# Optimization experiments

Measured on AMD Instinct MI355X. Metric: run time of the kernel, lower is better.

## Reference

```python
import jax, jax.numpy as jnp
import numpy as np

DT = 600.0          # integration time step (s)
STEPS = 20          # number of Euler steps
R_EARTH = 6371000.0
DEG2RAD = np.pi / 180.0
KERNEL = jnp.array([[1.0, 2.0, 1.0], [2.0, 4.0, 2.0], [1.0, 2.0, 1.0]], dtype=jnp.float32) / 16.0


def setup_inputs() -> dict:
    key = jax.random.key(0)
    kT, ku, kv, km = jax.random.split(key, 4)
    B, H, W = 8, 360, 720  # 0.5-degree global grid
    T = jax.random.normal(kT, (B, H, W), dtype=jnp.float32)
    ug = jax.random.normal(ku, (B, H, W), dtype=jnp.float32) * 0.5
    vg = jax.random.normal(kv, (B, H, W), dtype=jnp.float32) * 0.5
    lat = (90.0 - 0.25 - jnp.arange(H, dtype=jnp.float32) * 0.5)
    lon = jnp.arange(W, dtype=jnp.float32) * 0.5
    mask = (jax.random.uniform(km, (H, W)) > 0.3).astype(jnp.float32)  # ocean mask
    return {"T": T, "ug": ug, "vg": vg, "lat": lat, "lon": lon, "mask": mask}


def _horizontal_filter(field, mask):
    # field: (B, H, W); 3x3 binomial smoothing, zero ('valid'-style) padding=1, then mask
    k = KERNEL.reshape(1, 1, 3, 3).astype(field.dtype)
    f = jax.lax.conv_general_dilated(field[:, None, :, :], k, window_strides=(1, 1),
                                     padding=((1, 1), (1, 1)))
    return f[:, 0] * mask


def reference(T, ug, vg, lat, lon, mask):
    B, H, W = T.shape
    dlat = lat[1] - lat[0]
    dlon = lon[1] - lon[0]
    dy = R_EARTH * DEG2RAD * jnp.abs(dlat)
    sign_y = jnp.where(dlat > 0, 1.0, -1.0).astype(T.dtype)
    # dx varies with latitude: (H, 1) broadcasts over (B, H, W)
    dx = (R_EARTH * DEG2RAD * dlon) * jnp.cos(lat * DEG2RAD)[:, None]
    maskb = mask[None, :, :]

    def step(Tc, _):
        # boundary-aware meridional derivative
        top = (Tc[:, 1:2, :] - Tc[:, 0:1, :]) / dy
        bot = (Tc[:, -1:, :] - Tc[:, -2:-1, :]) / dy
        mid = (Tc[:, 2:, :] - Tc[:, :-2, :]) / (2.0 * dy)
        dT_dy = jnp.concatenate([top, mid, bot], axis=1) * sign_y
        # periodic zonal derivative
        dT_dx = (jnp.roll(Tc, -1, axis=2) - jnp.roll(Tc, 1, axis=2)) / (2.0 * dx)
        advection = ug * dT_dx + vg * dT_dy
        Tn = Tc - DT * advection * maskb  # Euler update with F = -advection*mask
        Tn = _horizontal_filter(Tn, maskb)
        return Tn, None

    T_final, _ = jax.lax.scan(step, T, None, length=STEPS)
    return T_final
```

## Files before the change

### kernel.cpp

```cpp
#include <hip/hip_runtime.h>

#define H 360
#define W 720
#define NB 8
#define XC 3
#define YC 10
#define TX 240
#define TY 36
#define BPB (XC*YC)
#define WR 52
#define LST 260
#define DTS 600.0f
#define REARTH 6371000.0f
#define D2R 0.017453292519943295f

#define NQ1 (WR*64)
#define NHALO 1168
#define NGROUPS 5
#define FLAG_STRIDE 32

static __device__ __forceinline__ float2 ldc8(const float* p) {
    unsigned long long u = __hip_atomic_load((const unsigned long long*)p,
                                             __ATOMIC_RELAXED, __HIP_MEMORY_SCOPE_AGENT);
    return __builtin_bit_cast(float2, u);
}
static __device__ __forceinline__ void stc8(float* p, float2 v) {
    __hip_atomic_store((unsigned long long*)p, __builtin_bit_cast(unsigned long long, v),
                       __ATOMIC_RELAXED, __HIP_MEMORY_SCOPE_AGENT);
}

__global__ __launch_bounds__(512, 2) void ocean_persist(
    const float* __restrict__ Tin, const float* __restrict__ ug,
    const float* __restrict__ vg, const float* __restrict__ lat,
    const float* __restrict__ lon, const float* __restrict__ mask,
    float* __restrict__ out, float* __restrict__ wsf, int* __restrict__ flags)
{
    __shared__ float sT[WR * LST];

    const int tid = threadIdx.x;
    const int b  = blockIdx.z;
    const int bx = blockIdx.x * TX;
    const int by = blockIdx.y * TY;
    const int plane = H * W;

    const float dlat = lat[1] - lat[0];
    const float dy   = REARTH * D2R * fabsf(dlat);
    const float sgn  = (dlat > 0.f) ? 1.f : -1.f;
    const float dlon = lon[1] - lon[0];
    const float i2dy = 0.5f / dy, i1dy = 1.f / dy;

    const float* Tb = Tin + b * plane;
    const float* ub = ug  + b * plane;
    const float* vb = vg  + b * plane;
    float* outb = out + b * plane;
    float* wsb  = wsf + b * plane;

    int* bflags = flags + b * BPB * FLAG_STRIDE;
    int* myflag = bflags + (blockIdx.y * XC + blockIdx.x) * FLAG_STRIDE;

    const int cq = tid & 63;
    const int rg = tid >> 6;
    const int c0 = cq << 2;
    const int a  = 1 + 6 * rg;
    const int gj0 = (bx - 8 + c0 + W) % W;
    const bool hlzb = (gj0 == 0);
    const bool hrzb = (gj0 + 3 == W - 1);
    const bool topB = (blockIdx.y == 0), botB = (blockIdx.y == YC - 1);

    int goff1[7], lds1o[7];
    #pragma unroll
    for (int k = 0; k < 7; ++k) {
        const int q = tid + 512 * k;
        if (q < NQ1) {
            const int r = q >> 6, cc0 = (q & 63) << 2;
            int gi = by - 8 + r; gi = min(max(gi, 0), H - 1);
            const int gj = (bx - 8 + cc0 + W) % W;
            goff1[k] = gi * W + gj;
            lds1o[k] = r * LST + cc0;
        } else goff1[k] = -1;
    }

    int hgo[3], hlo[3];
    #pragma unroll
    for (int t = 0; t < 3; ++t) {
        const int q = tid + 512 * t;
        if (q < NHALO) {
            int r, cc0;
            if (q < 1024) { const int ri = q >> 6; r = (ri < 8) ? ri : 36 + ri; cc0 = (q & 63) << 2; }
            else { const int u = q - 1024; r = 8 + (u >> 2); const int qi = u & 3;
                   cc0 = (qi < 2) ? (qi << 2) : (248 + ((qi - 2) << 2)); }
            int gi = by - 8 + r; gi = min(max(gi, 0), H - 1);
            const int gj = (bx - 8 + cc0 + W) % W;
            hgo[t] = gi * W + gj;
            hlo[t] = r * LST + cc0;
        } else hgo[t] = -1;
    }

    float cuA[8][4], cvA[8][4];
    unsigned domm = 0;
    #pragma unroll
    for (int j = 0; j < 8; ++j) {
        #pragma unroll
        for (int t = 0; t < 4; ++t) { cuA[j][t] = 0.f; cvA[j][t] = 0.f; }
        const int gi = by - 8 + a + j;
        if ((unsigned)gi < H) {
            const float dxv  = REARTH * D2R * dlon * cosf(lat[gi] * D2R);
            const float rdx2 = 0.5f / dxv;
            const float ivy  = (gi == 0 || gi == H - 1) ? i1dy : i2dy;
            #pragma unroll
            for (int t = 0; t < 4; ++t) {
                const int off = gi * W + gj0 + t;
                const float mk = mask[off];
                cuA[j][t] = -DTS * mk * ub[off] * rdx2;
                cvA[j][t] = -DTS * mk * vb[off] * sgn * ivy;
            }
            domm |= 1u << j;
        }
    }

    float m16A[6][4];
    int o3A[6];
    unsigned outm = 0, tilem = 0, ringm = 0;
    #pragma unroll
    for (int i = 0; i < 6; ++i) {
        const int n = 2 + 6 * rg + i;
        const int gi = by - 8 + n;
        o3A[i] = 0;
        #pragma unroll
        for (int t = 0; t < 4; ++t)
            m16A[i][t] = ((unsigned)gi < H) ? mask[gi * W + gj0 + t] * (1.f / 16.f) : 0.f;
        if ((unsigned)gi < H) outm |= 1u << i;
        const bool inTile = (n >= 8 && n <= 43 && cq >= 2 && cq <= 61);
        if (inTile) {
            o3A[i] = gi * W + bx + c0 - 8;
            tilem |= 1u << i;
            if (n <= 15 || n >= 36 || cq <= 3 || cq >= 60) ringm |= 1u << i;
        }
    }

    const int* nbrF = myflag;
    if (tid < 8) {
        int dyn, dxn;
        if (tid < 3)      { dyn = -1; dxn = tid - 1; }
        else if (tid == 3){ dyn = 0;  dxn = -1; }
        else if (tid == 4){ dyn = 0;  dxn = 1; }
        else              { dyn = 1;  dxn = tid - 6; }
        const int ny = (int)blockIdx.y + dyn;
        const int nx = ((int)blockIdx.x + dxn + XC) % XC;
        if (ny >= 0 && ny < YC) nbrF = bflags + (ny * XC + nx) * FLAG_STRIDE;
    }

    #pragma unroll
    for (int k = 0; k < 7; ++k)
        if (goff1[k] >= 0)
            *(float4*)(sT + lds1o[k]) = *(const float4*)(Tb + goff1[k]);
    __syncthreads();

    auto substep = [&](bool finalOut, float* ring) {
        float4 hA[8];
        float4 m1 = *(const float4*)(sT + (a - 1) * LST + c0);
        float4 cc = *(const float4*)(sT + a * LST + c0);
        #pragma unroll
        for (int j = 0; j < 8; ++j) {
            const float4 vD = *(const float4*)(sT + (a + j + 1) * LST + c0);
            const float tl = __shfl_up(cc.w, 1);
            const float tr = __shfl_down(cc.x, 1);
            const bool dj = (domm >> j) & 1;
            float4 o;
            o.x = (dj ? cc.x : 0.f) + cuA[j][0]*(cc.y - tl)   + cvA[j][0]*(vD.x - m1.x);
            o.y = (dj ? cc.y : 0.f) + cuA[j][1]*(cc.z - cc.x) + cvA[j][1]*(vD.y - m1.y);
            o.z = (dj ? cc.z : 0.f) + cuA[j][2]*(cc.w - cc.y) + cvA[j][2]*(vD.z - m1.z);
            o.w = (dj ? cc.w : 0.f) + cuA[j][3]*(tr   - cc.z) + cvA[j][3]*(vD.w - m1.w);
            float hl = __shfl_up(o.w, 1);
            float hr = __shfl_down(o.x, 1);
            if (hlzb) hl = 0.f;
            if (hrzb) hr = 0.f;
            hA[j].x = hl  + 2.f * o.x + o.y;
            hA[j].y = o.x + 2.f * o.y + o.z;
            hA[j].z = o.y + 2.f * o.z + o.w;
            hA[j].w = o.z + 2.f * o.w + hr;
            m1 = cc; cc = vD;
        }
        __syncthreads();
        #pragma unroll
        for (int i = 0; i < 6; ++i) {
            const float4 hm = hA[i], hc = hA[i + 1], hp = hA[i + 2];
            float4 o;
            o.x = (hm.x + 2.f * hc.x + hp.x) * m16A[i][0];
            o.y = (hm.y + 2.f * hc.y + hp.y) * m16A[i][1];
            o.z = (hm.z + 2.f * hc.z + hp.z) * m16A[i][2];
            o.w = (hm.w + 2.f * hc.w + hp.w) * m16A[i][3];
            if (!finalOut) {
                if ((outm >> i) & 1)
                    *(float4*)(sT + (2 + 6 * rg + i) * LST + c0) = o;
                if (topB && rg == 1 && i == 0) *(float4*)(sT + 7  * LST + c0) = o;
                if (botB && rg == 6 && i == 5) *(float4*)(sT + 44 * LST + c0) = o;
            } else if ((tilem >> i) & 1) {
                *(float4*)(outb + o3A[i]) = o;
            }
            if (ring && ((ringm >> i) & 1)) {
                float2 lo; lo.x = o.x; lo.y = o.y;
                float2 hi; hi.x = o.z; hi.y = o.w;
                stc8(ring + o3A[i], lo);
                stc8(ring + o3A[i] + 2, hi);
            }
        }
        __syncthreads();
    };

    #pragma unroll 1
    for (int g = 0; g < NGROUPS; ++g) {
        if (g) {
            __syncthreads();
            if (tid == 0)
                __hip_atomic_store(myflag, g, __ATOMIC_RELAXED, __HIP_MEMORY_SCOPE_AGENT);
            if (tid < 64) {
                long long t0 = (long long)clock64();
                for (;;) {
                    const int v = (tid < 8)
                        ? __hip_atomic_load(nbrF, __ATOMIC_RELAXED, __HIP_MEMORY_SCOPE_AGENT)
                        : 0x7fffffff;
                    if (__all(v >= g)) break;
                    __builtin_amdgcn_s_sleep(1);
                    if ((long long)clock64() - t0 > 200000000LL) break;
                }
            }
            __syncthreads();
            const float* prev = ((g - 1) & 1) ? wsb : outb;
            #pragma unroll
            for (int t = 0; t < 3; ++t) {
                if (hgo[t] >= 0) {
                    const float2 lo = ldc8(prev + hgo[t]);
                    const float2 hi = ldc8(prev + hgo[t] + 2);
                    float4 v; v.x = lo.x; v.y = lo.y; v.z = hi.x; v.w = hi.y;
                    *(float4*)(sT + hlo[t]) = v;
                }
            }
            __syncthreads();
        }
        const bool lastG = (g == NGROUPS - 1);
        float* ring = lastG ? nullptr : ((g & 1) ? wsb : outb);
        substep(false, nullptr);
        substep(false, nullptr);
        substep(false, nullptr);
        substep(lastG, ring);
    }
}

extern "C" void kernel_launch(void* const* d_in, const int* in_sizes, int n_in,
                              void* d_out, int out_size, void* d_ws, size_t ws_size,
                              hipStream_t stream)
{
    const float* T    = (const float*)d_in[0];
    const float* ug   = (const float*)d_in[1];
    const float* vg   = (const float*)d_in[2];
    const float* lat  = (const float*)d_in[3];
    const float* lon  = (const float*)d_in[4];
    const float* mask = (const float*)d_in[5];
    float* out = (float*)d_out;

    int*   flags = (int*)d_ws;
    float* wsf   = (float*)((char*)d_ws + 65536);

    hipMemsetAsync(d_ws, 0, 65536, stream);

    ocean_persist<<<dim3(XC, YC, NB), dim3(512), 0, stream>>>(
        T, ug, vg, lat, lon, mask, out, wsf, flags);
}
```

Baseline: 141.2 us.

## Halve tile height to double block count and occupancy in persistent kernel

Shrinks each block's tile from 36 to 18 rows, which doubles the grid to 20 row-blocks and raises launch bounds to 4 blocks per CU so more of the GPU is used concurrently. Per-thread register arrays shrink accordingly. Coefficient and mask loads are vectorised to float4. The ring exchange now writes every tile row instead of only edge rows, because with an 18-row tile the interior is small. The trade-off is a larger share of halo rows recomputed and more inter-block flag synchronisation per step.

```diff
diff --git a/kernel.cpp b/kernel.cpp
--- a/kernel.cpp
+++ b/kernel.cpp
@@ -4,18 +4,18 @@
 #define W 720
 #define NB 8
 #define XC 3
-#define YC 10
+#define YC 20
 #define TX 240
-#define TY 36
+#define TY 18
 #define BPB (XC*YC)
-#define WR 52
+#define WR 34
 #define LST 260
 #define DTS 600.0f
 #define REARTH 6371000.0f
 #define D2R 0.017453292519943295f
 
 #define NQ1 (WR*64)
-#define NHALO 1168
+#define NHALO 1096
 #define NGROUPS 5
 #define FLAG_STRIDE 32
 
@@ -29,7 +29,7 @@
                        __ATOMIC_RELAXED, __HIP_MEMORY_SCOPE_AGENT);
 }
 
-__global__ __launch_bounds__(512, 2) void ocean_persist(
+__global__ __launch_bounds__(512, 4) void ocean_persist(
     const float* __restrict__ Tin, const float* __restrict__ ug,
     const float* __restrict__ vg, const float* __restrict__ lat,
     const float* __restrict__ lon, const float* __restrict__ mask,
@@ -61,15 +61,15 @@
     const int cq = tid & 63;
     const int rg = tid >> 6;
     const int c0 = cq << 2;
-    const int a  = 1 + 6 * rg;
+    const int a  = 1 + 4 * rg;
     const int gj0 = (bx - 8 + c0 + W) % W;
     const bool hlzb = (gj0 == 0);
     const bool hrzb = (gj0 + 3 == W - 1);
     const bool topB = (blockIdx.y == 0), botB = (blockIdx.y == YC - 1);
 
-    int goff1[7], lds1o[7];
-    #pragma unroll
-    for (int k = 0; k < 7; ++k) {
+    int goff1[5], lds1o[5];
+    #pragma unroll
+    for (int k = 0; k < 5; ++k) {
         const int q = tid + 512 * k;
         if (q < NQ1) {
             const int r = q >> 6, cc0 = (q & 63) << 2;
@@ -86,7 +86,7 @@
         const int q = tid + 512 * t;
         if (q < NHALO) {
             int r, cc0;
-            if (q < 1024) { const int ri = q >> 6; r = (ri < 8) ? ri : 36 + ri; cc0 = (q & 63) << 2; }
+            if (q < 1024) { const int ri = q >> 6; r = (ri < 8) ? ri : 18 + ri; cc0 = (q & 63) << 2; }
             else { const int u = q - 1024; r = 8 + (u >> 2); const int qi = u & 3;
                    cc0 = (qi < 2) ? (qi << 2) : (248 + ((qi - 2) << 2)); }
             int gi = by - 8 + r; gi = min(max(gi, 0), H - 1);
@@ -96,45 +96,57 @@
         } else hgo[t] = -1;
     }
 
-    float cuA[8][4], cvA[8][4];
+    float cuA[6][4], cvA[6][4];
     unsigned domm = 0;
     #pragma unroll
-    for (int j = 0; j < 8; ++j) {
+    for (int j = 0; j < 6; ++j) {
         #pragma unroll
         for (int t = 0; t < 4; ++t) { cuA[j][t] = 0.f; cvA[j][t] = 0.f; }
-        const int gi = by - 8 + a + j;
-        if ((unsigned)gi < H) {
+        const int hr = a + j;
+        const int gi = by - 8 + hr;
+        if (hr <= 32 && (unsigned)gi < H) {
             const float dxv  = REARTH * D2R * dlon * cosf(lat[gi] * D2R);
             const float rdx2 = 0.5f / dxv;
             const float ivy  = (gi == 0 || gi == H - 1) ? i1dy : i2dy;
-            #pragma unroll
-            for (int t = 0; t < 4; ++t) {
-                const int off = gi * W + gj0 + t;
-                const float mk = mask[off];
-                cuA[j][t] = -DTS * mk * ub[off] * rdx2;
-                cvA[j][t] = -DTS * mk * vb[off] * sgn * ivy;
-            }
+            const int base = gi * W + gj0;
+            const float4 mk4 = *(const float4*)(mask + base);
+            const float4 u4  = *(const float4*)(ub + base);
+            const float4 v4  = *(const float4*)(vb + base);
+            cuA[j][0] = -DTS * mk4.x * u4.x * rdx2;
+            cuA[j][1] = -DTS * mk4.y * u4.y * rdx2;
+            cuA[j][2] = -DTS * mk4.z * u4.z * rdx2;
+            cuA[j][3] = -DTS * mk4.w * u4.w * rdx2;
+            const float cs = sgn * ivy;
+            cvA[j][0] = -DTS * mk4.x * v4.x * cs;
+            cvA[j][1] = -DTS * mk4.y * v4.y * cs;
+            cvA[j][2] = -DTS * mk4.z * v4.z * cs;
+            cvA[j][3] = -DTS * mk4.w * v4.w * cs;
             domm |= 1u << j;
         }
     }
 
-    float m16A[6][4];
-    int o3A[6];
-    unsigned outm = 0, tilem = 0, ringm = 0;
-    #pragma unroll
-    for (int i = 0; i < 6; ++i) {
-        const int n = 2 + 6 * rg + i;
+    float m16A[4][4];
+    int o3A[4];
+    unsigned outm = 0, tilem = 0;
+    #pragma unroll
+    for (int i = 0; i < 4; ++i) {
+        const int n = 2 + 4 * rg + i;
         const int gi = by - 8 + n;
         o3A[i] = 0;
         #pragma unroll
-        for (int t = 0; t < 4; ++t)
-            m16A[i][t] = ((unsigned)gi < H) ? mask[gi * W + gj0 + t] * (1.f / 16.f) : 0.f;
-        if ((unsigned)gi < H) outm |= 1u << i;
-        const bool inTile = (n >= 8 && n <= 43 && cq >= 2 && cq <= 61);
+        for (int t = 0; t < 4; ++t) m16A[i][t] = 0.f;
+        if ((unsigned)gi < H) {
+            const float4 mk4 = *(const float4*)(mask + gi * W + gj0);
+            m16A[i][0] = mk4.x * (1.f / 16.f);
+            m16A[i][1] = mk4.y * (1.f / 16.f);
+            m16A[i][2] = mk4.z * (1.f / 16.f);
+            m16A[i][3] = mk4.w * (1.f / 16.f);
+            if (n <= 31) outm |= 1u << i;
+        }
+        const bool inTile = (n >= 8 && n <= 25 && cq >= 2 && cq <= 61);
         if (inTile) {
             o3A[i] = gi * W + bx + c0 - 8;
             tilem |= 1u << i;
-            if (n <= 15 || n >= 36 || cq <= 3 || cq >= 60) ringm |= 1u << i;
         }
     }
 
@@ -151,18 +163,19 @@
     }
 
     #pragma unroll
-    for (int k = 0; k < 7; ++k)
+    for (int k = 0; k < 5; ++k)
         if (goff1[k] >= 0)
             *(float4*)(sT + lds1o[k]) = *(const float4*)(Tb + goff1[k]);
     __syncthreads();
 
     auto substep = [&](bool finalOut, float* ring) {
-        float4 hA[8];
+        float4 hA[6];
         float4 m1 = *(const float4*)(sT + (a - 1) * LST + c0);
         float4 cc = *(const float4*)(sT + a * LST + c0);
         #pragma unroll
-        for (int j = 0; j < 8; ++j) {
-            const float4 vD = *(const float4*)(sT + (a + j + 1) * LST + c0);
+        for (int j = 0; j < 6; ++j) {
+            const int rD = min(a + j + 1, WR - 1);
+            const float4 vD = *(const float4*)(sT + rD * LST + c0);
             const float tl = __shfl_up(cc.w, 1);
             const float tr = __shfl_down(cc.x, 1);
             const bool dj = (domm >> j) & 1;
@@ -183,7 +196,7 @@
         }
         __syncthreads();
         #pragma unroll
-        for (int i = 0; i < 6; ++i) {
+        for (int i = 0; i < 4; ++i) {
             const float4 hm = hA[i], hc = hA[i + 1], hp = hA[i + 2];
             float4 o;
             o.x = (hm.x + 2.f * hc.x + hp.x) * m16A[i][0];
@@ -192,13 +205,13 @@
             o.w = (hm.w + 2.f * hc.w + hp.w) * m16A[i][3];
             if (!finalOut) {
                 if ((outm >> i) & 1)
-                    *(float4*)(sT + (2 + 6 * rg + i) * LST + c0) = o;
-                if (topB && rg == 1 && i == 0) *(float4*)(sT + 7  * LST + c0) = o;
-                if (botB && rg == 6 && i == 5) *(float4*)(sT + 44 * LST + c0) = o;
+                    *(float4*)(sT + (2 + 4 * rg + i) * LST + c0) = o;
+                if (topB && rg == 1 && i == 2) *(float4*)(sT + 7  * LST + c0) = o;
+                if (botB && rg == 5 && i == 3) *(float4*)(sT + 26 * LST + c0) = o;
             } else if ((tilem >> i) & 1) {
                 *(float4*)(outb + o3A[i]) = o;
             }
-            if (ring && ((ringm >> i) & 1)) {
+            if (ring && ((tilem >> i) & 1)) {
                 float2 lo; lo.x = o.x; lo.y = o.y;
                 float2 hi; hi.x = o.z; hi.y = o.w;
                 stc8(ring + o3A[i], lo);
```

Result: slower. 212.6 us (+50.6%).
